# Kernel tuning notes

Measured on AMD Instinct MI355X. Metric: run time of the kernel, lower is better.

Reference implementation:

```python
import jax, jax.numpy as jnp
import numpy as np

H, E, D, S, B = 16, 1024, 64, 2048, 4  # heads, emb, head_size, seq_len, batch

def setup_inputs() -> dict:
    key = jax.random.key(0)
    ks = jax.random.split(key, 9)
    sc_e = 1.0 / np.sqrt(E)
    sc_hd = 1.0 / np.sqrt(H * D)
    return {
        "x":  jax.random.normal(ks[0], (B, S, E), dtype=jnp.float32),
        # per-head q/k/v projection weights, stacked: [H, E, D]
        "Wq": jax.random.uniform(ks[1], (H, E, D), jnp.float32, -sc_e, sc_e),
        "Wk": jax.random.uniform(ks[2], (H, E, D), jnp.float32, -sc_e, sc_e),
        "Wv": jax.random.uniform(ks[3], (H, E, D), jnp.float32, -sc_e, sc_e),
        "bq": jax.random.uniform(ks[4], (H, D), jnp.float32, -sc_e, sc_e),
        "bk": jax.random.uniform(ks[5], (H, D), jnp.float32, -sc_e, sc_e),
        "bv": jax.random.uniform(ks[6], (H, D), jnp.float32, -sc_e, sc_e),
        # output projection: Linear(H*D -> E)
        "Wo": jax.random.uniform(ks[7], (H * D, E), jnp.float32, -sc_hd, sc_hd),
        "bo": jax.random.uniform(ks[8], (E,), jnp.float32, -sc_hd, sc_hd),
    }

def reference(x, Wq, Wk, Wv, bq, bk, bv, Wo, bo):
    b, s, e = x.shape
    # batched per-head projections: [B, H, S, D]
    q = jnp.einsum("bse,hed->bhsd", x, Wq) + bq[None, :, None, :]
    k = jnp.einsum("bse,hed->bhsd", x, Wk) + bk[None, :, None, :]
    v = jnp.einsum("bse,hed->bhsd", x, Wv) + bv[None, :, None, :]
    scale = 1.0 / jnp.sqrt(jnp.asarray(q.shape[-1], q.dtype))
    scores = jnp.einsum("bhqd,bhkd->bhqk", q, k) * scale  # [B,H,S,S]
    causal = jnp.tril(jnp.ones((s, s), dtype=bool))
    scores = jnp.where(causal[None, None], scores, jnp.asarray(-jnp.inf, scores.dtype))
    attn = jax.nn.softmax(scores, axis=-1)
    heads = jnp.einsum("bhqk,bhkd->bhqd", attn, v)  # [B,H,S,D]
    concat = heads.transpose(0, 2, 1, 3).reshape(b, s, -1)  # [B,S,H*D]
    return concat @ Wo + bo  # dropout is identity at inference
```

## Files before the change

kernel.cpp:

```cpp
#include <hip/hip_runtime.h>
#include <hip/hip_bf16.h>

#define H_ 16
#define E_ 1024
#define D_ 64
#define S_ 2048
#define B_ 4
#define M_ (B_ * S_)

typedef __bf16 bf16_t;
typedef __bf16 bf16x8 __attribute__((ext_vector_type(8)));
typedef __bf16 bf16x4 __attribute__((ext_vector_type(4)));
typedef float f32x4 __attribute__((ext_vector_type(4)));

typedef __attribute__((address_space(1))) unsigned int gu32;
typedef __attribute__((address_space(3))) unsigned int lu32;

__device__ __forceinline__ f32x4 mfma16(bf16x8 a, bf16x8 b, f32x4 c) {
  return __builtin_amdgcn_mfma_f32_16x16x32_bf16(a, b, c, 0, 0, 0);
}
__device__ __forceinline__ void gl2lds16(const bf16_t* g, bf16_t* l) {
  __builtin_amdgcn_global_load_lds((const gu32*)g, (lu32*)l, 16, 0, 0);
}

#define BAR() asm volatile("s_barrier" ::: "memory")

__device__ __forceinline__ int detect_f32(const unsigned short* __restrict__ xu) {
  int lane = threadIdx.x & 63;
  int cnt = 0;
  for (int i = 0; i < 4; ++i) {
    unsigned short v = xu[(lane * 4 + i) * 2];
    cnt += __popcll(__ballot(((v >> 7) & 0xFF) >= 0xC0));
  }
  return cnt > 16;
}

__global__ __launch_bounds__(256) void convert_x(
    const void* __restrict__ src, bf16_t* __restrict__ dst,
    int* __restrict__ flag, long n) {
  const int f32 = detect_f32((const unsigned short*)src);
  if (blockIdx.x == 0 && threadIdx.x == 0) { flag[0] = f32; flag[1] = 0; }
  long i = ((long)blockIdx.x * 256 + threadIdx.x) * 8;
  if (i >= n) return;
  bf16x8 v;
  if (f32) {
    const float* s = (const float*)src;
    for (int j = 0; j < 8; ++j) v[j] = (bf16_t)s[i + j];
  } else {
    v = *(const bf16x8*)((const bf16_t*)src + i);
  }
  *(bf16x8*)(dst + i) = v;
}

__global__ __launch_bounds__(256) void transpose_w(
    const void* __restrict__ s0, const void* __restrict__ s1,
    const void* __restrict__ s2, const void* __restrict__ s3,
    bf16_t* __restrict__ d0, bf16_t* __restrict__ d1,
    bf16_t* __restrict__ d2, bf16_t* __restrict__ d3,
    const int* __restrict__ flag) {
  __shared__ __align__(16) bf16_t tile[64][72];
  const int f32 = *flag;
  const int z = blockIdx.z;
  const int t = threadIdx.x;
  const void* src_;
  bf16_t* dst;
  long sOff;
  int N, K, tk, tn;
  if (z < 3) {
    const int h = blockIdx.y;
    src_ = z == 0 ? s0 : (z == 1 ? s1 : s2);
    dst = (z == 0 ? d0 : (z == 1 ? d1 : d2)) + (long)h * E_ * D_;
    sOff = (long)h * E_ * D_;
    N = D_; K = E_;
    tk = blockIdx.x * 64; tn = 0;
  } else {
    src_ = s3; dst = d3; sOff = 0;
    N = E_; K = E_;
    tk = blockIdx.x * 64; tn = blockIdx.y * 64;
  }
  for (int i = 0; i < 2; ++i) {
    int c = t + i * 256;
    int r = c >> 3, col = (c & 7) * 8;
    if (f32) {
      const float* s = (const float*)src_ + sOff;
      const float* p = &s[(long)(tk + r) * N + tn + col];
      for (int j = 0; j < 8; ++j) tile[r][col + j] = (bf16_t)p[j];
    } else {
      const bf16_t* s = (const bf16_t*)src_ + sOff;
      *(bf16x8*)&tile[r][col] = *(const bf16x8*)&s[(long)(tk + r) * N + tn + col];
    }
  }
  __syncthreads();
  for (int i = 0; i < 2; ++i) {
    int c = t + i * 256;
    int r = c >> 3, col = (c & 7) * 8;
    bf16x8 v;
    for (int j = 0; j < 8; ++j) v[j] = tile[col + j][r];
    *(bf16x8*)&dst[(long)(tn + r) * K + tk + col] = v;
  }
}

template <int NBF, int KIND>
__global__ __launch_bounds__(512, 2) void gemm8(
    const bf16_t* __restrict__ A, const bf16_t* __restrict__ Bt,
    const void* __restrict__ bias0, const void* __restrict__ bias1,
    const void* __restrict__ bias2,
    bf16_t* __restrict__ Cq, void* __restrict__ Cout,
    const int* __restrict__ flag) {
  __shared__ __align__(16) bf16_t LA[2 * 256 * 64];
  __shared__ __align__(16) bf16_t LB[2 * NBF * 64 * 64];
  const int t = threadIdx.x;
  const int wave = t >> 6, lane = t & 63;
  const int quad = lane >> 4, l16 = lane & 15;
  const int wm = (wave >> 2) * 128;
  const int wn = (wave & 3) * (NBF * 16);
  const int bid = blockIdx.x;
  const int xcd = bid & 7, l = bid >> 3;
  const int m0 = (xcd * 4 + (l & 3)) * 256;
  const int n0 = (l >> 2) * (NBF * 64);

  f32x4 acc[8][NBF] = {};

  const int sr = lane >> 3;
  const int sj = ((lane & 7) ^ sr) << 3;
  auto stA = [&](int u, int tt, int buf) {
    bf16_t* lp = &LA[buf * 16384 + u * 4096 + wave * 512];
    if constexpr (KIND == 0) {
      gl2lds16(&A[(long)(m0 + u * 64 + wave * 8 + sr) * 1024 + tt * 64 + sj], lp);
    } else {
      int m = m0 + u * 64 + wave * 8 + sr;
      int b = m >> 11, s = m & (S_ - 1);
      gl2lds16(&A[(((long)(b * H_ + tt)) * S_ + s) * D_ + sj], lp);
    }
  };
  auto stB = [&](int u, int tt, int buf) {
    bf16_t* lp = &LB[buf * (NBF * 4096) + u * 4096 + wave * 512];
    gl2lds16(&Bt[(long)(n0 + u * 64 + wave * 8 + sr) * 1024 + tt * 64 + sj], lp);
  };
  auto stage = [&](int tt, int buf) {
    stB(0, tt, buf); stB(1, tt, buf);
    if constexpr (NBF == 3) stB(2, tt, buf);
    stA(0, tt, buf); stA(1, tt, buf); stA(2, tt, buf); stA(3, tt, buf);
  };

  auto rdA = [&](int buf, int i, int kk) {
    int R = wm + i * 16 + l16;
    return *(const bf16x8*)&LA[buf * 16384 + R * 64 + (((kk * 4 + quad) ^ (R & 7)) << 3)];
  };
  auto rdB = [&](int buf, int j, int kk) {
    int R = wn + j * 16 + l16;
    return *(const bf16x8*)&LB[buf * (NBF * 4096) + R * 64 + (((kk * 4 + quad) ^ (R & 7)) << 3)];
  };
  auto compute = [&](int buf) {
    bf16x8 a0[8], a1[8], b0[NBF], b1[NBF];
#pragma unroll
    for (int j = 0; j < NBF; ++j) b0[j] = rdB(buf, j, 0);
#pragma unroll
    for (int i = 0; i < 8; ++i) a0[i] = rdA(buf, i, 0);
#pragma unroll
    for (int j = 0; j < NBF; ++j) b1[j] = rdB(buf, j, 1);
#pragma unroll
    for (int i = 0; i < 8; ++i) a1[i] = rdA(buf, i, 1);
    __builtin_amdgcn_s_setprio(1);
#pragma unroll
    for (int i = 0; i < 8; ++i)
#pragma unroll
      for (int j = 0; j < NBF; ++j)
        acc[i][j] = mfma16(b0[j], a0[i], acc[i][j]);
#pragma unroll
    for (int i = 0; i < 8; ++i)
#pragma unroll
      for (int j = 0; j < NBF; ++j)
        acc[i][j] = mfma16(b1[j], a1[i], acc[i][j]);
    __builtin_amdgcn_s_setprio(0);
  };

  stage(0, 0);

#pragma unroll 1
  for (int tt = 0; tt < 14; tt += 2) {
    stage(tt + 1, 1);
    asm volatile("s_waitcnt vmcnt(%0)" :: "n"(NBF + 4) : "memory");
    BAR();
    compute(0);
    BAR();
    stage(tt + 2, 0);
    asm volatile("s_waitcnt vmcnt(%0)" :: "n"(NBF + 4) : "memory");
    BAR();
    compute(1);
    BAR();
  }
  stage(15, 1);
  asm volatile("s_waitcnt vmcnt(%0)" :: "n"(NBF + 4) : "memory");
  BAR();
  compute(0);
  BAR();
  asm volatile("s_waitcnt vmcnt(0)" ::: "memory");
  BAR();
  compute(1);

  const int f32io = flag[0];
  if constexpr (KIND == 0) {
#pragma unroll
    for (int i = 0; i < 8; ++i) {
      const int m = m0 + wm + i * 16 + l16;
      const int b = m >> 11, s = m & (S_ - 1);
#pragma unroll
      for (int j = 0; j < NBF; ++j) {
        const int n = n0 + wn + j * 16 + quad * 4;
        const int which = n >> 10, nin = n & 1023;
        const int h = nin >> 6, d = nin & 63;
        const void* bp = which == 0 ? bias0 : (which == 1 ? bias1 : bias2);
        if (which == 2) {
          bf16_t* Vt = Cq + 2L * ((long)B_ * H_ * S_ * D_);
#pragma unroll
          for (int r = 0; r < 4; ++r) {
            float bv = f32io ? ((const float*)bp)[nin + r]
                             : (float)((const bf16_t*)bp)[nin + r];
            Vt[(((long)(b * H_ + h)) * D_ + d + r) * S_ + s] =
                (bf16_t)(acc[i][j][r] + bv);
          }
        } else {
          bf16x4 o;
#pragma unroll
          for (int r = 0; r < 4; ++r) {
            float bv = f32io ? ((const float*)bp)[nin + r]
                             : (float)((const bf16_t*)bp)[nin + r];
            o[r] = (bf16_t)(acc[i][j][r] + bv);
          }
          *(bf16x4*)&Cq[(long)which * (B_ * H_ * S_ * D_) +
                        (((long)(b * H_ + h)) * S_ + s) * D_ + d] = o;
        }
      }
    }
  } else {
#pragma unroll
    for (int i = 0; i < 8; ++i) {
      const long m = m0 + wm + i * 16 + l16;
#pragma unroll
      for (int j = 0; j < NBF; ++j) {
        const int n = n0 + wn + j * 16 + quad * 4;
        if (f32io) {
          f32x4 o;
#pragma unroll
          for (int r = 0; r < 4; ++r)
            o[r] = acc[i][j][r] + ((const float*)bias0)[n + r];
          *(f32x4*)&((float*)Cout)[m * 1024 + n] = o;
        } else {
          bf16x4 o;
#pragma unroll
          for (int r = 0; r < 4; ++r)
            o[r] = (bf16_t)(acc[i][j][r] + (float)((const bf16_t*)bias0)[n + r]);
          *(bf16x4*)&((bf16_t*)Cout)[m * 1024 + n] = o;
        }
      }
    }
  }
}

__global__ __launch_bounds__(256) void attn_k(
    bf16_t* QO,
    const bf16_t* __restrict__ Kg_,
    const bf16_t* __restrict__ Vtg_) {
  __shared__ __align__(16) bf16_t Ks[64 * 64];
  __shared__ __align__(16) bf16_t Vs[64 * 64];
  __shared__ __align__(16) bf16_t Pq[4][32 * 72];
  const int t = threadIdx.x;
  const int wave = t >> 6, lane = t & 63;
  const int quad = lane >> 4, l16 = lane & 15;
  const int bid = blockIdx.x;
  const int qb = 15 - (bid >> 6);
  const int bh = bid & 63;
  const long base = (long)bh * S_ * D_;
  bf16_t* Qg = QO + base;
  const bf16_t* Kg = Kg_ + base;
  const bf16_t* Vt = Vtg_ + base;
  const int q0 = qb * 128, qrl = wave * 32;
  const int rot = ((lane & 7) - (lane >> 3)) & 7;

  bf16x8 qf[2][2];
  for (int n = 0; n < 2; ++n) {
    long row = q0 + qrl + n * 16 + l16;
    bf16x8 a = *(const bf16x8*)&Qg[row * D_ + quad * 8];
    bf16x8 b = *(const bf16x8*)&Qg[row * D_ + 32 + quad * 8];
    for (int j = 0; j < 8; ++j) {
      a[j] = (bf16_t)((float)a[j] * 0.18033688f);
      b[j] = (bf16_t)((float)b[j] * 0.18033688f);
    }
    qf[n][0] = a; qf[n][1] = b;
  }
  bf16x8 ones;
  for (int j = 0; j < 8; ++j) ones[j] = (bf16_t)1.0f;
  f32x4 o_acc[2][4] = {};
  f32x4 lacc[2] = {};

  const int nkt = 2 * qb + 2;
  for (int kt = 0; kt < nkt; ++kt) {
    __syncthreads();
    for (int i = 0; i < 2; ++i) {
      int c = wave * 2 + i;
      gl2lds16(&Kg[(long)(kt * 64 + c * 8 + (lane >> 3)) * D_ + rot * 8],
               &Ks[c * 512]);
      gl2lds16(&Vt[(long)(c * 8 + (lane >> 3)) * S_ + kt * 64 + rot * 8],
               &Vs[c * 512]);
    }
    __syncthreads();

    if (kt * 64 > q0 + qrl + 31) continue;

    f32x4 sc[2][4];
    for (int mt = 0; mt < 4; ++mt) {
      int krow = mt * 16 + l16;
      bf16x8 kf0 = *(const bf16x8*)&Ks[krow * 64 + (((quad + krow) & 7) << 3)];
      bf16x8 kf1 = *(const bf16x8*)&Ks[krow * 64 + (((quad + 4 + krow) & 7) << 3)];
      for (int n = 0; n < 2; ++n) {
        f32x4 z = {0.f, 0.f, 0.f, 0.f};
        z = mfma16(kf0, qf[n][0], z);
        z = mfma16(kf1, qf[n][1], z);
        sc[n][mt] = z;
      }
    }
    if (kt * 64 + 63 > q0 + qrl) {
      for (int n = 0; n < 2; ++n) {
        int qr = q0 + qrl + n * 16 + l16;
        for (int mt = 0; mt < 4; ++mt)
          for (int r = 0; r < 4; ++r) {
            int kc = kt * 64 + mt * 16 + quad * 4 + r;
            if (kc > qr) sc[n][mt][r] = -1e30f;
          }
      }
    }
    for (int n = 0; n < 2; ++n)
      for (int mt = 0; mt < 4; ++mt) {
        bf16x4 pb;
        for (int r = 0; r < 4; ++r)
          pb[r] = (bf16_t)__builtin_amdgcn_exp2f(sc[n][mt][r]);
        *(bf16x4*)&Pq[wave][(n * 16 + l16) * 72 + mt * 16 + quad * 4] = pb;
      }
    bf16x8 pf[2][2];
    for (int m = 0; m < 2; ++m) {
      pf[m][0] = *(const bf16x8*)&Pq[wave][(m * 16 + l16) * 72 + quad * 8];
      pf[m][1] = *(const bf16x8*)&Pq[wave][(m * 16 + l16) * 72 + 32 + quad * 8];
    }
    for (int m = 0; m < 2; ++m) {
      lacc[m] = mfma16(pf[m][0], ones, lacc[m]);
      lacc[m] = mfma16(pf[m][1], ones, lacc[m]);
    }
    for (int dt = 0; dt < 4; ++dt) {
      int drow = dt * 16 + l16;
      bf16x8 vf0 = *(const bf16x8*)&Vs[drow * 64 + (((quad + drow) & 7) << 3)];
      bf16x8 vf1 = *(const bf16x8*)&Vs[drow * 64 + (((quad + 4 + drow) & 7) << 3)];
      for (int m = 0; m < 2; ++m) {
        o_acc[m][dt] = mfma16(pf[m][0], vf0, o_acc[m][dt]);
        o_acc[m][dt] = mfma16(pf[m][1], vf1, o_acc[m][dt]);
      }
    }
  }
  for (int m = 0; m < 2; ++m)
    for (int r = 0; r < 4; ++r) {
      float inv = 1.0f / lacc[m][r];
      long qg = q0 + qrl + m * 16 + quad * 4 + r;
      for (int dt = 0; dt < 4; ++dt)
        Qg[qg * D_ + dt * 16 + l16] = (bf16_t)(o_acc[m][dt][r] * inv);
    }
}

extern "C" void kernel_launch(void* const* d_in, const int* in_sizes, int n_in,
                              void* d_out, int out_size, void* d_ws, size_t ws_size,
                              hipStream_t stream) {
  (void)in_sizes; (void)n_in; (void)out_size; (void)ws_size;
  const void* x  = d_in[0];
  const void* Wq = d_in[1];
  const void* Wk = d_in[2];
  const void* Wv = d_in[3];
  const void* bq = d_in[4];
  const void* bk = d_in[5];
  const void* bv = d_in[6];
  const void* Wo = d_in[7];
  const void* bo = d_in[8];

  char* base = (char*)d_ws;
  int* flag = (int*)base;
  bf16_t* p = (bf16_t*)(base + 16);
  bf16_t* xb_ = p; p += (size_t)M_ * E_;
  bf16_t* qo_ = p; p += (size_t)B_ * H_ * S_ * D_;
  bf16_t* kb_ = p; p += (size_t)B_ * H_ * S_ * D_;
  bf16_t* vb_ = p; p += (size_t)B_ * H_ * S_ * D_;
  bf16_t* wqt = p; p += (size_t)H_ * D_ * E_;
  bf16_t* wkt = p; p += (size_t)H_ * D_ * E_;
  bf16_t* wvt = p; p += (size_t)H_ * D_ * E_;
  bf16_t* wot = p; p += (size_t)E_ * E_;

  convert_x<<<(M_ * E_) / (256 * 8), 256, 0, stream>>>(x, xb_, flag, (long)M_ * E_);

  transpose_w<<<dim3(16, 16, 4), 256, 0, stream>>>(
      Wq, Wk, Wv, Wo, wqt, wkt, wvt, wot, flag);

  gemm8<3, 0><<<dim3(512), 512, 0, stream>>>(
      xb_, wqt, bq, bk, bv, qo_, nullptr, flag);

  attn_k<<<dim3(1024), 256, 0, stream>>>(qo_, kb_, vb_);

  gemm8<2, 1><<<dim3(256), 512, 0, stream>>>(
      qo_, wot, bo, nullptr, nullptr, nullptr, d_out, flag);
}
```

Measured before the change: 274.9 us.

## Merge x conversion and weight transpose into one prep kernel; stage V transpose via LDS

Combines the x fp32-to-bf16 conversion and the weight transpose into a single launch, with each block doing its own format detection, which removes one kernel launch and its gap. In the QKV GEMM epilogue, V outputs are first written transposed into shared memory and then stored to the transposed V buffer as coalesced 16-byte rows. The old path wrote scattered 2-byte elements with stride S. The cost is extra LDS traffic and barriers, and the shared buffer is reused from the GEMM tiles.

After: 261.1 us. 5.0% less time.

```diff
diff --git a/kernel.cpp b/kernel.cpp
--- a/kernel.cpp
+++ b/kernel.cpp
@@ -35,48 +35,47 @@
   return cnt > 16;
 }
 
-__global__ __launch_bounds__(256) void convert_x(
-    const void* __restrict__ src, bf16_t* __restrict__ dst,
-    int* __restrict__ flag, long n) {
-  const int f32 = detect_f32((const unsigned short*)src);
-  if (blockIdx.x == 0 && threadIdx.x == 0) { flag[0] = f32; flag[1] = 0; }
-  long i = ((long)blockIdx.x * 256 + threadIdx.x) * 8;
-  if (i >= n) return;
-  bf16x8 v;
-  if (f32) {
-    const float* s = (const float*)src;
-    for (int j = 0; j < 8; ++j) v[j] = (bf16_t)s[i + j];
-  } else {
-    v = *(const bf16x8*)((const bf16_t*)src + i);
-  }
-  *(bf16x8*)(dst + i) = v;
-}
-
-__global__ __launch_bounds__(256) void transpose_w(
+__global__ __launch_bounds__(256) void prep(
+    const void* __restrict__ x,
     const void* __restrict__ s0, const void* __restrict__ s1,
     const void* __restrict__ s2, const void* __restrict__ s3,
+    bf16_t* __restrict__ xb,
     bf16_t* __restrict__ d0, bf16_t* __restrict__ d1,
     bf16_t* __restrict__ d2, bf16_t* __restrict__ d3,
-    const int* __restrict__ flag) {
+    int* __restrict__ flag, long n) {
   __shared__ __align__(16) bf16_t tile[64][72];
-  const int f32 = *flag;
-  const int z = blockIdx.z;
+  const int f32 = detect_f32((const unsigned short*)x);
+  const int bid = blockIdx.x;
   const int t = threadIdx.x;
+  if (bid >= 1024) {
+    if (bid == 1024 && t == 0) { flag[0] = f32; flag[1] = 0; }
+    long i = ((long)(bid - 1024) * 256 + t) * 8;
+    if (i >= n) return;
+    bf16x8 v;
+    if (f32) {
+      const float* s = (const float*)x;
+      for (int j = 0; j < 8; ++j) v[j] = (bf16_t)s[i + j];
+    } else {
+      v = *(const bf16x8*)((const bf16_t*)x + i);
+    }
+    *(bf16x8*)(xb + i) = v;
+    return;
+  }
+  const int z = bid >> 8, y = (bid >> 4) & 15, xt = bid & 15;
   const void* src_;
   bf16_t* dst;
   long sOff;
   int N, K, tk, tn;
   if (z < 3) {
-    const int h = blockIdx.y;
     src_ = z == 0 ? s0 : (z == 1 ? s1 : s2);
-    dst = (z == 0 ? d0 : (z == 1 ? d1 : d2)) + (long)h * E_ * D_;
-    sOff = (long)h * E_ * D_;
+    dst = (z == 0 ? d0 : (z == 1 ? d1 : d2)) + (long)y * E_ * D_;
+    sOff = (long)y * E_ * D_;
     N = D_; K = E_;
-    tk = blockIdx.x * 64; tn = 0;
+    tk = xt * 64; tn = 0;
   } else {
     src_ = s3; dst = d3; sOff = 0;
     N = E_; K = E_;
-    tk = blockIdx.x * 64; tn = blockIdx.y * 64;
+    tk = xt * 64; tn = y * 64;
   }
   for (int i = 0; i < 2; ++i) {
     int c = t + i * 256;
@@ -107,8 +106,9 @@
     const void* __restrict__ bias2,
     bf16_t* __restrict__ Cq, void* __restrict__ Cout,
     const int* __restrict__ flag) {
-  __shared__ __align__(16) bf16_t LA[2 * 256 * 64];
-  __shared__ __align__(16) bf16_t LB[2 * NBF * 64 * 64];
+  __shared__ __align__(16) char LSmem[65536 + NBF * 16384];
+  bf16_t* LA = (bf16_t*)LSmem;
+  bf16_t* LB = (bf16_t*)(LSmem + 65536);
   const int t = threadIdx.x;
   const int wave = t >> 6, lane = t & 63;
   const int quad = lane >> 4, l16 = lane & 15;
@@ -201,26 +201,29 @@
 
   const int f32io = flag[0];
   if constexpr (KIND == 0) {
+    BAR();
+    bf16_t* Vl = (bf16_t*)LSmem;
+    const int nv0 = 2048 - n0;
 #pragma unroll
     for (int i = 0; i < 8; ++i) {
       const int m = m0 + wm + i * 16 + l16;
       const int b = m >> 11, s = m & (S_ - 1);
+      const int sloc = wm + i * 16 + l16;
 #pragma unroll
       for (int j = 0; j < NBF; ++j) {
-        const int n = n0 + wn + j * 16 + quad * 4;
+        const int nf = wn + j * 16;
+        const int n = n0 + nf + quad * 4;
         const int which = n >> 10, nin = n & 1023;
-        const int h = nin >> 6, d = nin & 63;
         const void* bp = which == 0 ? bias0 : (which == 1 ? bias1 : bias2);
-        if (which == 2) {
-          bf16_t* Vt = Cq + 2L * ((long)B_ * H_ * S_ * D_);
+        if (nf >= nv0) {
 #pragma unroll
           for (int r = 0; r < 4; ++r) {
             float bv = f32io ? ((const float*)bp)[nin + r]
                              : (float)((const bf16_t*)bp)[nin + r];
-            Vt[(((long)(b * H_ + h)) * D_ + d + r) * S_ + s] =
-                (bf16_t)(acc[i][j][r] + bv);
+            Vl[(nf + quad * 4 + r) * 264 + sloc] = (bf16_t)(acc[i][j][r] + bv);
           }
         } else {
+          const int h = nin >> 6, d = nin & 63;
           bf16x4 o;
 #pragma unroll
           for (int r = 0; r < 4; ++r) {
@@ -231,6 +234,19 @@
           *(bf16x4*)&Cq[(long)which * (B_ * H_ * S_ * D_) +
                         (((long)(b * H_ + h)) * S_ + s) * D_ + d] = o;
         }
+      }
+    }
+    if (nv0 < 192) {
+      BAR();
+      bf16_t* Vt = Cq + 2L * ((long)B_ * H_ * S_ * D_);
+      const int b = m0 >> 11, sbase = m0 & (S_ - 1);
+      const int rv0 = nv0 > 0 ? nv0 : 0;
+      const int eo = (t & 31) * 8;
+      for (int row = rv0 + (t >> 5); row < 192; row += 16) {
+        const int nin = n0 + row - 2048;
+        const int h = nin >> 6, d = nin & 63;
+        bf16x8 v = *(const bf16x8*)&Vl[row * 264 + eo];
+        *(bf16x8*)&Vt[(((long)(b * H_ + h)) * D_ + d) * S_ + sbase + eo] = v;
       }
     }
   } else {
@@ -391,10 +407,8 @@
   bf16_t* wvt = p; p += (size_t)H_ * D_ * E_;
   bf16_t* wot = p; p += (size_t)E_ * E_;
 
-  convert_x<<<(M_ * E_) / (256 * 8), 256, 0, stream>>>(x, xb_, flag, (long)M_ * E_);
-
-  transpose_w<<<dim3(16, 16, 4), 256, 0, stream>>>(
-      Wq, Wk, Wv, Wo, wqt, wkt, wvt, wot, flag);
+  prep<<<dim3(1024 + (M_ * E_) / (256 * 8)), 256, 0, stream>>>(
+      x, Wq, Wk, Wv, Wo, xb_, wqt, wkt, wvt, wot, flag, (long)M_ * E_);
 
   gemm8<3, 0><<<dim3(512), 512, 0, stream>>>(
       xb_, wqt, bq, bk, bv, qo_, nullptr, flag);
```
